# Performance work log

Measured on AMD Instinct MI355X. Metric: run time of the kernel, lower is better.

## Reference

```python
import jax, jax.numpy as jnp
import numpy as np

P, U, N = 1024, 196, 2048
B, T = 4, 512
D_IN, D_H, D_OUT = 384, 512, 256
NH, HD, TOPK = 4, 64, 64
EPS = 1e-5


def _ln(x, g, b):
    m = jnp.mean(x, axis=-1, keepdims=True)
    v = jnp.var(x, axis=-1, keepdims=True)
    return (x - m) * jax.lax.rsqrt(v + EPS) * g + b


def setup_inputs() -> dict:
    key = jax.random.key(0)
    k = jax.random.split(key, 12)
    s = 0.05
    return {
        'patches': jax.random.normal(k[0], (P, U, D_IN), jnp.float32),
        'patch_ids': jax.random.randint(k[1], (N,), 0, P),
        'valid_mask': jnp.ones((B, T), dtype=bool),
        'patch_center_gps': jax.random.normal(k[2], (N, 2), jnp.float32),
        'offsets': jax.random.randint(k[3], (N, 2), 0, 14),
        'W1': jax.random.normal(k[4], (D_IN, D_H), jnp.float32) * s,
        'b1': jnp.zeros((D_H,), jnp.float32),
        'W2': jax.random.normal(k[5], (D_H, D_OUT), jnp.float32) * s,
        'b2': jnp.zeros((D_OUT,), jnp.float32),
        'ln_q_g': jnp.ones((D_OUT,), jnp.float32),
        'ln_q_b': jnp.zeros((D_OUT,), jnp.float32),
        'ln_kv_g': jnp.ones((D_OUT,), jnp.float32),
        'ln_kv_b': jnp.zeros((D_OUT,), jnp.float32),
        'Wq': jax.random.normal(k[6], (D_OUT, D_OUT), jnp.float32) * s,
        'bq': jnp.zeros((D_OUT,), jnp.float32),
        'Wk': jax.random.normal(k[7], (D_OUT, D_OUT), jnp.float32) * s,
        'bk': jnp.zeros((D_OUT,), jnp.float32),
        'Wv': jax.random.normal(k[8], (D_OUT, D_OUT), jnp.float32) * s,
        'bv': jnp.zeros((D_OUT,), jnp.float32),
        'Wo': jax.random.normal(k[9], (D_OUT, D_OUT), jnp.float32) * s,
        'bo': jnp.zeros((D_OUT,), jnp.float32),
    }


def reference(patches, patch_ids, valid_mask, patch_center_gps, offsets,
              W1, b1, W2, b2, ln_q_g, ln_q_b, ln_kv_g, ln_kv_b,
              Wq, bq, Wk, bk, Wv, bv, Wo, bo):
    # gather patch feature grids per valid cell: [N, U, D_IN]
    gathered = patches[patch_ids]
    # adapter MLP (dropout is identity at eval)
    h = gathered @ W1 + b1
    h = jnp.where(h >= 0, h, 0.01 * h)  # LeakyReLU(0.01)
    a = h @ W2 + b2                      # [N, U, D_OUT]
    # offset-indexed query patch within the HxW grid
    Hs = int(np.sqrt(U)); Ws = Hs; ci = Hs // 2; cj = Ws // 2
    i_t = jnp.clip(ci + offsets[:, 1], 0, Hs - 1)
    j_t = jnp.clip(cj + offsets[:, 0], 0, Ws - 1)
    idx = (i_t * Ws + j_t).astype(jnp.int32)             # [N]
    query = jnp.take_along_axis(a, idx[:, None, None], axis=1)[:, 0]  # [N, D_OUT]
    # cosine similarity (F.normalize uses eps=1e-12 clamp on the norm)
    qn = query / jnp.clip(jnp.linalg.norm(query, axis=-1, keepdims=True), 1e-12)
    an = a / jnp.clip(jnp.linalg.norm(a, axis=-1, keepdims=True), 1e-12)
    sim = jnp.einsum('nd,nud->nu', qn, an)               # [N, U]
    _, topi = jax.lax.top_k(sim, TOPK)                   # [N, TOPK]
    kv = jnp.take_along_axis(a, topi[:, :, None], axis=1)  # [N, TOPK, D_OUT]
    # LayerNorm on q and kv, then multi-head cross-attention (1 query token)
    qln = _ln(query, ln_q_g, ln_q_b)
    kvln = _ln(kv, ln_kv_g, ln_kv_b)
    q = (qln @ Wq + bq).reshape(-1, NH, HD)              # [N, H, Hd]
    kk = (kvln @ Wk + bk).reshape(-1, TOPK, NH, HD)
    vv = (kvln @ Wv + bv).reshape(-1, TOPK, NH, HD)
    scores = jnp.einsum('nhd,nkhd->nhk', q, kk) / np.float32(np.sqrt(HD))
    w = jax.nn.softmax(scores, axis=-1)
    o = jnp.einsum('nhk,nkhd->nhd', w, vv).reshape(-1, D_OUT)
    attn = o @ Wo + bo                                   # [N, D_OUT]
    # masked scatter into [B, T, D_OUT] (row-major order of valid cells)
    mflat = valid_mask.reshape(-1)
    pos = jnp.cumsum(mflat.astype(jnp.int32)) - 1
    gath = attn[jnp.clip(pos, 0, attn.shape[0] - 1)]
    grid = jnp.where(mflat[:, None], gath, 0.0)
    return grid.reshape(valid_mask.shape[0], valid_mask.shape[1], D_OUT)
```

## Files before the change

kernel.cpp:

```cpp
#include <hip/hip_runtime.h>
#include <hip/hip_bf16.h>
#include <stdint.h>

#define NCELL 2048
#define UG    196
#define DIN   384
#define DH    512
#define DOUT  256
#define EPSV  1e-5f

typedef _Float16 f16;
typedef _Float16 f16x4 __attribute__((ext_vector_type(4)));
typedef _Float16 f16x8 __attribute__((ext_vector_type(8)));
typedef float    f32x16 __attribute__((ext_vector_type(16)));
typedef unsigned short ushortx4 __attribute__((ext_vector_type(4)));

#define AB_BYTES   205520896ull
#define QRAW_OFF   AB_BYTES
#define SIM_OFF    (QRAW_OFF + 2097152ull)
#define QNORM_OFF  (SIM_OFF + 1605632ull)
#define W1F_OFF    (QNORM_OFF + 8192ull)
#define W1F_BYTES  786432ull
#define W2F_OFF    (W1F_OFF + W1F_BYTES)
#define W2F_BYTES  524288ull

__global__ __launch_bounds__(256)
void k_prep(const float* __restrict__ W1, const float* __restrict__ W2,
            f16* __restrict__ w1f, f16* __restrict__ w2f)
{
    const int c = blockIdx.x * 256 + threadIdx.x;
    if (c < 49152) {
        const int lane = c & 63;
        const int part = (c >> 6) & 1;
        const int cg   = (c >> 7) & 7;
        const int half = (c >> 10) & 1;
        const int ks   = c >> 11;
        const int col  = (half * 8 + cg) * 32 + (lane & 31);
        const int kb   = ks * 16 + (lane >> 5) * 8;
        f16x8 o;
        #pragma unroll
        for (int j = 0; j < 8; ++j) {
            const float wv = W1[(size_t)(kb + j) * DH + col];
            const f16 hi = (f16)wv;
            o[j] = (part == 0) ? hi : (f16)(wv - (float)hi);
        }
        *(f16x8*)(w1f + (size_t)c * 8) = o;
    } else if (c < 81920) {
        const int c2 = c - 49152;
        const int lane = c2 & 63;
        const int part = (c2 >> 6) & 1;
        const int cg   = (c2 >> 7) & 7;
        const int ks   = c2 >> 10;
        const int col  = cg * 32 + (lane & 31);
        const int kb   = ks * 16 + (lane >> 5) * 8;
        f16x8 o;
        #pragma unroll
        for (int j = 0; j < 8; ++j) {
            const float wv = W2[(size_t)(kb + j) * DOUT + col];
            const f16 hi = (f16)wv;
            o[j] = (part == 0) ? hi : (f16)(wv - (float)hi);
        }
        *(f16x8*)(w2f + (size_t)c2 * 8) = o;
    }
}

__global__ __launch_bounds__(256)
void k_query(const float* __restrict__ patches, const int* __restrict__ patch_ids,
             const int* __restrict__ offsets,
             const float* __restrict__ W1, const float* __restrict__ b1,
             const float* __restrict__ W2, const float* __restrict__ b2,
             float* __restrict__ qraw, float* __restrict__ qnorm)
{
    __shared__ float sA[8 * DIN];
    __shared__ float sH[8 * DH];
    __shared__ float sPart[4 * 8];
    __shared__ int   sSrc[8];
    const int t  = threadIdx.x;
    const int nb = blockIdx.x * 8;
    if (t < 8) {
        int n  = nb + t;
        int ox = offsets[2 * n + 0];
        int oy = offsets[2 * n + 1];
        int it = min(max(7 + oy, 0), 13);
        int jt = min(max(7 + ox, 0), 13);
        sSrc[t] = patch_ids[n] * 196 + it * 14 + jt;
    }
    __syncthreads();
    #pragma unroll
    for (int i = 0; i < 3; ++i) {
        int fi = t + 256 * i;
        int r = fi / 96, c4 = fi % 96;
        const float4 v = ((const float4*)(patches + (size_t)sSrc[r] * DIN))[c4];
        ((float4*)(sA + r * DIN))[c4] = v;
    }
    __syncthreads();
    float h0[8], h1[8];
    {
        const float bb0 = b1[t], bb1 = b1[t + 256];
        #pragma unroll
        for (int r = 0; r < 8; ++r) { h0[r] = bb0; h1[r] = bb1; }
    }
    for (int k = 0; k < DIN; ++k) {
        const float w0 = W1[k * DH + t];
        const float w1 = W1[k * DH + t + 256];
        #pragma unroll
        for (int r = 0; r < 8; ++r) {
            const float av = sA[r * DIN + k];
            h0[r] = fmaf(av, w0, h0[r]);
            h1[r] = fmaf(av, w1, h1[r]);
        }
    }
    #pragma unroll
    for (int r = 0; r < 8; ++r) {
        float v0 = h0[r]; v0 = v0 >= 0.f ? v0 : 0.01f * v0;
        float v1 = h1[r]; v1 = v1 >= 0.f ? v1 : 0.01f * v1;
        sH[r * DH + t]       = v0;
        sH[r * DH + t + 256] = v1;
    }
    __syncthreads();
    float a8[8];
    {
        const float bb = b2[t];
        #pragma unroll
        for (int r = 0; r < 8; ++r) a8[r] = bb;
    }
    for (int k = 0; k < DH; ++k) {
        const float w = W2[k * DOUT + t];
        #pragma unroll
        for (int r = 0; r < 8; ++r) a8[r] = fmaf(sH[r * DH + k], w, a8[r]);
    }
    const int wid = t >> 6;
    #pragma unroll
    for (int r = 0; r < 8; ++r) {
        float p = a8[r] * a8[r];
        #pragma unroll
        for (int m = 1; m < 64; m <<= 1) p += __shfl_xor(p, m);
        if ((t & 63) == 0) sPart[wid * 8 + r] = p;
    }
    __syncthreads();
    if (t < 8) {
        float s = sPart[t] + sPart[8 + t] + sPart[16 + t] + sPart[24 + t];
        qnorm[nb + t] = fmaxf(sqrtf(s), 1e-12f);
    }
    #pragma unroll
    for (int r = 0; r < 8; ++r)
        qraw[(size_t)(nb + r) * DOUT + t] = a8[r];
}

__global__ __launch_bounds__(256)
void k_mlp(const float* __restrict__ patches, const int* __restrict__ patch_ids,
           const f16* __restrict__ w1f, const f16* __restrict__ w2f,
           const float* __restrict__ b1, const float* __restrict__ b2,
           const float* __restrict__ qraw, const float* __restrict__ qnorm,
           __hip_bfloat16* __restrict__ ab, float* __restrict__ sims)
{
    __shared__ __align__(16) unsigned char sAH[65536];
    __shared__ float sRed[256];
    const int t  = threadIdx.x;
    const int w  = t >> 6;
    const int l  = t & 63;
    const int R0 = blockIdx.x * 32;

    {
        const int row = t >> 3;
        const int Rg  = R0 + row;
        const int n   = Rg / UG, u = Rg - n * UG;
        const float* srcrow = patches + ((size_t)patch_ids[n] * UG + u) * DIN;
        const int swz = (row & 7) << 4;
        #pragma unroll
        for (int c = 0; c < 12; ++c) {
            const int k0 = (t & 7) * 4 + c * 32;
            const float4 v = *(const float4*)(srcrow + k0);
            f16x4 hi, lo;
            hi[0] = (f16)v.x; lo[0] = (f16)(v.x - (float)hi[0]);
            hi[1] = (f16)v.y; lo[1] = (f16)(v.y - (float)hi[1]);
            hi[2] = (f16)v.z; lo[2] = (f16)(v.z - (float)hi[2]);
            hi[3] = (f16)v.w; lo[3] = (f16)(v.w - (float)hi[3]);
            const int boff = row * 768 + ((k0 * 2) ^ swz);
            *(f16x4*)(sAH + boff)         = hi;
            *(f16x4*)(sAH + 24576 + boff) = lo;
        }
    }
    __syncthreads();

    f32x16 acc1[2][2];
    #pragma unroll
    for (int h = 0; h < 2; ++h)
        #pragma unroll
        for (int c = 0; c < 2; ++c)
            #pragma unroll
            for (int r = 0; r < 16; ++r) acc1[h][c][r] = 0.f;

    const int row  = l & 31;
    const int swzr = (row & 7) << 4;
    const f16* wb1 = w1f + (2 * w) * 1024 + l * 8;
    const f16* wb2 = w2f + (2 * w) * 1024 + l * 8;

#define LOADB(dst, base, s)                                   \
    {                                                         \
        const f16* bp_ = (base) + (size_t)(s) * 8192;         \
        dst##0 = *(const f16x8*)(bp_);                        \
        dst##1 = *(const f16x8*)(bp_ + 512);                  \
        dst##2 = *(const f16x8*)(bp_ + 1024);                 \
        dst##3 = *(const f16x8*)(bp_ + 1536);                 \
    }

#define STAGE1(s, B)                                                                  \
    {                                                                                 \
        const int ks_ = (s) >> 1, h_ = (s) & 1;                                       \
        const int aoff_ = row * 768 + ((ks_ * 32 + (l >> 5) * 16) ^ swzr);            \
        const f16x8 a_h = *(const f16x8*)(sAH + aoff_);                               \
        const f16x8 a_l = *(const f16x8*)(sAH + 24576 + aoff_);                       \
        acc1[h_][0] = __builtin_amdgcn_mfma_f32_32x32x16_f16(a_h, B##0, acc1[h_][0], 0, 0, 0); \
        acc1[h_][1] = __builtin_amdgcn_mfma_f32_32x32x16_f16(a_h, B##2, acc1[h_][1], 0, 0, 0); \
        acc1[h_][0] = __builtin_amdgcn_mfma_f32_32x32x16_f16(a_h, B##1, acc1[h_][0], 0, 0, 0); \
        acc1[h_][1] = __builtin_amdgcn_mfma_f32_32x32x16_f16(a_h, B##3, acc1[h_][1], 0, 0, 0); \
        acc1[h_][0] = __builtin_amdgcn_mfma_f32_32x32x16_f16(a_l, B##0, acc1[h_][0], 0, 0, 0); \
        acc1[h_][1] = __builtin_amdgcn_mfma_f32_32x32x16_f16(a_l, B##2, acc1[h_][1], 0, 0, 0); \
    }

    {
        f16x8 bA0, bA1, bA2, bA3, bB0, bB1, bB2, bB3;
        LOADB(bA, wb1, 0)
        for (int s2 = 0; s2 < 24; ++s2) {
            LOADB(bB, wb1, 2 * s2 + 1)
            STAGE1(2 * s2, bA)
            if (s2 < 23) LOADB(bA, wb1, 2 * s2 + 2)
            STAGE1(2 * s2 + 1, bB)
        }
    }
    __syncthreads();

    {
        #pragma unroll
        for (int h = 0; h < 2; ++h)
            #pragma unroll
            for (int c = 0; c < 2; ++c) {
                const int col = (h * 8 + 2 * w + c) * 32 + (l & 31);
                const float bb = b1[col];
                #pragma unroll
                for (int r = 0; r < 16; ++r) {
                    const int rw = (r & 3) + 8 * (r >> 2) + 4 * (l >> 5);
                    float v = acc1[h][c][r] + bb;
                    v = v >= 0.f ? v : 0.01f * v;
                    const f16 hh = (f16)v;
                    const f16 hl = (f16)(v - (float)hh);
                    const int boff = rw * 1024 + ((col * 2) ^ ((rw & 7) << 4));
                    *(f16*)(sAH + boff)         = hh;
                    *(f16*)(sAH + 32768 + boff) = hl;
                }
            }
    }
    __syncthreads();

    f32x16 acc2[2];
    #pragma unroll
    for (int c = 0; c < 2; ++c)
        #pragma unroll
        for (int r = 0; r < 16; ++r) acc2[c][r] = 0.f;

#define STAGE2(s, B)                                                                  \
    {                                                                                 \
        const int hoff_ = row * 1024 + (((s) * 32 + (l >> 5) * 16) ^ swzr);           \
        const f16x8 h_h = *(const f16x8*)(sAH + hoff_);                               \
        const f16x8 h_l = *(const f16x8*)(sAH + 32768 + hoff_);                       \
        acc2[0] = __builtin_amdgcn_mfma_f32_32x32x16_f16(h_h, B##0, acc2[0], 0, 0, 0); \
        acc2[1] = __builtin_amdgcn_mfma_f32_32x32x16_f16(h_h, B##2, acc2[1], 0, 0, 0); \
        acc2[0] = __builtin_amdgcn_mfma_f32_32x32x16_f16(h_h, B##1, acc2[0], 0, 0, 0); \
        acc2[1] = __builtin_amdgcn_mfma_f32_32x32x16_f16(h_h, B##3, acc2[1], 0, 0, 0); \
        acc2[0] = __builtin_amdgcn_mfma_f32_32x32x16_f16(h_l, B##0, acc2[0], 0, 0, 0); \
        acc2[1] = __builtin_amdgcn_mfma_f32_32x32x16_f16(h_l, B##2, acc2[1], 0, 0, 0); \
    }

    {
        f16x8 bA0, bA1, bA2, bA3, bB0, bB1, bB2, bB3;
        LOADB(bA, wb2, 0)
        for (int s2 = 0; s2 < 16; ++s2) {
            LOADB(bB, wb2, 2 * s2 + 1)
            STAGE2(2 * s2, bA)
            if (s2 < 15) LOADB(bA, wb2, 2 * s2 + 2)
            STAGE2(2 * s2 + 1, bB)
        }
    }
#undef LOADB
#undef STAGE1
#undef STAGE2

    float* sRedN = sRed;
    float* sRedD = sRed + 128;
    {
        float nrm[16], dot[16];
        #pragma unroll
        for (int r = 0; r < 16; ++r) { nrm[r] = 0.f; dot[r] = 0.f; }
        #pragma unroll
        for (int c = 0; c < 2; ++c) {
            const int col = (2 * w + c) * 32 + (l & 31);
            const float bb = b2[col];
            #pragma unroll
            for (int r = 0; r < 16; ++r) {
                const int rw = (r & 3) + 8 * (r >> 2) + 4 * (l >> 5);
                const int Rg = R0 + rw;
                const int n  = Rg / UG;
                const float a = acc2[c][r] + bb;
                const float q = qraw[(size_t)n * DOUT + col];
                nrm[r] = fmaf(a, a, nrm[r]);
                dot[r] = fmaf(a, q, dot[r]);
                ab[(size_t)Rg * DOUT + col] = __float2bfloat16(a);
            }
        }
        #pragma unroll
        for (int r = 0; r < 16; ++r) {
            #pragma unroll
            for (int m = 1; m < 32; m <<= 1) {
                nrm[r] += __shfl_xor(nrm[r], m);
                dot[r] += __shfl_xor(dot[r], m);
            }
        }
        if ((l & 31) == 0) {
            #pragma unroll
            for (int r = 0; r < 16; ++r) {
                const int rw = (r & 3) + 8 * (r >> 2) + 4 * (l >> 5);
                sRedN[rw * 4 + w] = nrm[r];
                sRedD[rw * 4 + w] = dot[r];
            }
        }
    }
    __syncthreads();
    if (t < 32) {
        const float nrm = sRedN[t * 4] + sRedN[t * 4 + 1] + sRedN[t * 4 + 2] + sRedN[t * 4 + 3];
        const float dot = sRedD[t * 4] + sRedD[t * 4 + 1] + sRedD[t * 4 + 2] + sRedD[t * 4 + 3];
        const int Rg = R0 + t, n = Rg / UG;
        sims[Rg] = dot / (qnorm[n] * fmaxf(sqrtf(nrm), 1e-12f));
    }
}

__global__ __launch_bounds__(256)
void k_attn(const __hip_bfloat16* __restrict__ ab,
            const float* __restrict__ qraw,
            const float* __restrict__ sims,
            const float* __restrict__ lnqg, const float* __restrict__ lnqb,
            const float* __restrict__ lnkg, const float* __restrict__ lnkb,
            const float* __restrict__ Wq, const float* __restrict__ bq,
            const float* __restrict__ Wk, const float* __restrict__ bk,
            const float* __restrict__ Wv, const float* __restrict__ bv,
            const float* __restrict__ Wo, const float* __restrict__ bo,
            float* __restrict__ out)
{
    __shared__ float sKV[64 * 257];
    __shared__ float ssim[256];
    __shared__ int   sflag[256];
    __shared__ int   ssel[64];
    __shared__ __align__(16) float sQln[256];
    __shared__ __align__(16) float sQp[256];
    __shared__ float sQw[4 * 256];
    __shared__ float sWatt[256];
    __shared__ float sWkv[4 * 256];
    __shared__ float sO[256];
    __shared__ float sred[8];

    const int t = threadIdx.x;
    const int n = blockIdx.x;
    (void)bk;

    ssim[t] = (t < 196) ? sims[(size_t)n * 196 + t] : -3.0e38f;
    const float qv = qraw[(size_t)n * DOUT + t];
    float s1 = qv, s2 = qv * qv;
    #pragma unroll
    for (int m = 1; m < 64; m <<= 1) { s1 += __shfl_xor(s1, m); s2 += __shfl_xor(s2, m); }
    if ((t & 63) == 0) { sred[t >> 6] = s1; sred[4 + (t >> 6)] = s2; }
    __syncthreads();
    {
        const float mean = (sred[0] + sred[1] + sred[2] + sred[3]) * (1.f / 256.f);
        const float var  = (sred[4] + sred[5] + sred[6] + sred[7]) * (1.f / 256.f) - mean * mean;
        sQln[t] = (qv - mean) * rsqrtf(var + EPSV) * lnqg[t] + lnqb[t];
    }
    int flag = 0;
    if (t < 196) {
        const float su = ssim[t];
        int rank = 0;
        for (int v = 0; v < 196; ++v) {
            const float sv = ssim[v];
            rank += (sv > su) || (sv == su && v < t);
        }
        flag = (rank < 64) ? 1 : 0;
    }
    sflag[t] = flag;
    __syncthreads();
    if (flag) {
        int pos = 0;
        for (int v = 0; v < t; ++v) pos += sflag[v];
        ssel[pos] = t;
    }
    __syncthreads();

    {
        float acc = bq[t];
        for (int k = 0; k < 256; ++k)
            acc = fmaf(sQln[k], Wq[k * DOUT + t], acc);
        sQp[t] = acc;
    }

    {
        const int s = t >> 2;
        const int q = t & 3;
        const int u = ssel[s];
        const unsigned short* src =
            (const unsigned short*)(ab + ((size_t)n * 196 + u) * (size_t)DOUT);
        float sum = 0.f, ssq = 0.f;
        #pragma unroll
        for (int i = 0; i < 16; ++i) {
            const int c = q * 4 + i * 16;
            const ushortx4 rv = *(const ushortx4*)(src + c);
            #pragma unroll
            for (int j = 0; j < 4; ++j) {
                const float f = __builtin_bit_cast(float, (unsigned)rv[j] << 16);
                sKV[s * 257 + c + j] = f;
                sum += f; ssq = fmaf(f, f, ssq);
            }
        }
        sum += __shfl_xor(sum, 1); ssq += __shfl_xor(ssq, 1);
        sum += __shfl_xor(sum, 2); ssq += __shfl_xor(ssq, 2);
        const float mean = sum * (1.f / 256.f);
        const float inv  = rsqrtf(ssq * (1.f / 256.f) - mean * mean + EPSV);
        #pragma unroll
        for (int i = 0; i < 16; ++i) {
            const int c = q * 4 + i * 16;
            const float4 g = *(const float4*)(lnkg + c);
            const float4 b = *(const float4*)(lnkb + c);
            float x0 = sKV[s * 257 + c + 0], x1 = sKV[s * 257 + c + 1];
            float x2 = sKV[s * 257 + c + 2], x3 = sKV[s * 257 + c + 3];
            sKV[s * 257 + c + 0] = (x0 - mean) * inv * g.x + b.x;
            sKV[s * 257 + c + 1] = (x1 - mean) * inv * g.y + b.y;
            sKV[s * 257 + c + 2] = (x2 - mean) * inv * g.z + b.z;
            sKV[s * 257 + c + 3] = (x3 - mean) * inv * g.w + b.w;
        }
    }
    __syncthreads();

    {
        const float* wrow = Wk + (size_t)t * DOUT;
        #pragma unroll
        for (int h = 0; h < 4; ++h) {
            float acc = 0.f;
            #pragma unroll
            for (int d4 = 0; d4 < 16; ++d4) {
                const float4 wv = *(const float4*)(wrow + h * 64 + d4 * 4);
                const float4 qp = *(const float4*)(sQp + h * 64 + d4 * 4);
                acc = fmaf(qp.x, wv.x, acc);
                acc = fmaf(qp.y, wv.y, acc);
                acc = fmaf(qp.z, wv.z, acc);
                acc = fmaf(qp.w, wv.w, acc);
            }
            sQw[h * 256 + t] = acc;
        }
    }
    __syncthreads();

    {
        const int h = t >> 6, s = t & 63;
        float acc = 0.f;
        for (int k = 0; k < 256; ++k)
            acc = fmaf(sKV[s * 257 + k], sQw[h * 256 + k], acc);
        float sc = acc * 0.125f;
        float mx = sc;
        #pragma unroll
        for (int m = 1; m < 64; m <<= 1) mx = fmaxf(mx, __shfl_xor(mx, m));
        const float e = expf(sc - mx);
        float sum = e;
        #pragma unroll
        for (int m = 1; m < 64; m <<= 1) sum += __shfl_xor(sum, m);
        sWatt[t] = e / sum;
    }
    __syncthreads();

    {
        float a0 = 0.f, a1 = 0.f, a2 = 0.f, a3 = 0.f;
        for (int s = 0; s < 64; ++s) {
            const float kvv = sKV[s * 257 + t];
            a0 = fmaf(sWatt[s], kvv, a0);
            a1 = fmaf(sWatt[64 + s], kvv, a1);
            a2 = fmaf(sWatt[128 + s], kvv, a2);
            a3 = fmaf(sWatt[192 + s], kvv, a3);
        }
        sWkv[t] = a0; sWkv[256 + t] = a1; sWkv[512 + t] = a2; sWkv[768 + t] = a3;
    }
    __syncthreads();

    {
        const int h = t >> 6;
        float acc = bv[t];
        for (int k = 0; k < 256; ++k)
            acc = fmaf(sWkv[h * 256 + k], Wv[k * DOUT + t], acc);
        sO[t] = acc;
    }
    __syncthreads();

    {
        float acc = bo[t];
        for (int k = 0; k < 256; ++k)
            acc = fmaf(sO[k], Wo[k * DOUT + t], acc);
        out[(size_t)n * DOUT + t] = acc;
    }
}

extern "C" void kernel_launch(void* const* d_in, const int* in_sizes, int n_in,
                              void* d_out, int out_size, void* d_ws, size_t ws_size,
                              hipStream_t stream) {
    (void)in_sizes; (void)n_in; (void)out_size; (void)ws_size;
    const float* patches   = (const float*)d_in[0];
    const int*   patch_ids = (const int*)d_in[1];
    const int*   offsets   = (const int*)d_in[4];
    const float* W1 = (const float*)d_in[5];
    const float* b1 = (const float*)d_in[6];
    const float* W2 = (const float*)d_in[7];
    const float* b2 = (const float*)d_in[8];
    const float* lnqg = (const float*)d_in[9];
    const float* lnqb = (const float*)d_in[10];
    const float* lnkg = (const float*)d_in[11];
    const float* lnkb = (const float*)d_in[12];
    const float* Wq = (const float*)d_in[13];
    const float* bq = (const float*)d_in[14];
    const float* Wk = (const float*)d_in[15];
    const float* bk = (const float*)d_in[16];
    const float* Wv = (const float*)d_in[17];
    const float* bv = (const float*)d_in[18];
    const float* Wo = (const float*)d_in[19];
    const float* bo = (const float*)d_in[20];

    uint8_t* ws = (uint8_t*)d_ws;
    __hip_bfloat16* ab    = (__hip_bfloat16*)(ws);
    float*          qraw  = (float*)(ws + QRAW_OFF);
    float*          sims  = (float*)(ws + SIM_OFF);
    float*          qnorm = (float*)(ws + QNORM_OFF);
    f16*            w1f   = (f16*)(ws + W1F_OFF);
    f16*            w2f   = (f16*)(ws + W2F_OFF);
    float*          out   = (float*)d_out;

    hipLaunchKernelGGL(k_prep, dim3(320), dim3(256), 0, stream, W1, W2, w1f, w2f);
    hipLaunchKernelGGL(k_query, dim3(NCELL / 8), dim3(256), 0, stream,
                       patches, patch_ids, offsets, W1, b1, W2, b2, qraw, qnorm);
    hipLaunchKernelGGL(k_mlp, dim3((NCELL * UG) / 32), dim3(256), 0, stream,
                       patches, patch_ids, w1f, w2f, b1, b2, qraw, qnorm, ab, sims);
    hipLaunchKernelGGL(k_attn, dim3(NCELL), dim3(256), 0, stream,
                       ab, qraw, sims, lnqg, lnqb, lnkg, lnkb,
                       Wq, bq, Wk, bk, Wv, bv, Wo, bo, out);
}
```

Baseline: 1.212 ms.

## Use 8 waves per k_mlp block, halving per-wave column tiles

Measured after the change: 1.127 ms. -7.0%, faster.

```diff
diff --git a/kernel.cpp b/kernel.cpp
--- a/kernel.cpp
+++ b/kernel.cpp
@@ -147,7 +147,7 @@
         qraw[(size_t)(nb + r) * DOUT + t] = a8[r];
 }
 
-__global__ __launch_bounds__(256)
+__global__ __launch_bounds__(512)
 void k_mlp(const float* __restrict__ patches, const int* __restrict__ patch_ids,
            const f16* __restrict__ w1f, const f16* __restrict__ w2f,
            const float* __restrict__ b1, const float* __restrict__ b2,
@@ -155,21 +155,21 @@
            __hip_bfloat16* __restrict__ ab, float* __restrict__ sims)
 {
     __shared__ __align__(16) unsigned char sAH[65536];
-    __shared__ float sRed[256];
+    __shared__ float sRed[512];
     const int t  = threadIdx.x;
     const int w  = t >> 6;
     const int l  = t & 63;
     const int R0 = blockIdx.x * 32;
 
     {
-        const int row = t >> 3;
+        const int row = t >> 4;
         const int Rg  = R0 + row;
         const int n   = Rg / UG, u = Rg - n * UG;
         const float* srcrow = patches + ((size_t)patch_ids[n] * UG + u) * DIN;
         const int swz = (row & 7) << 4;
         #pragma unroll
-        for (int c = 0; c < 12; ++c) {
-            const int k0 = (t & 7) * 4 + c * 32;
+        for (int c = 0; c < 6; ++c) {
+            const int k0 = (t & 15) * 4 + c * 64;
             const float4 v = *(const float4*)(srcrow + k0);
             f16x4 hi, lo;
             hi[0] = (f16)v.x; lo[0] = (f16)(v.x - (float)hi[0]);
@@ -181,132 +181,127 @@
             *(f16x4*)(sAH + 24576 + boff) = lo;
         }
     }
-    __syncthreads();
-
-    f32x16 acc1[2][2];
-    #pragma unroll
-    for (int h = 0; h < 2; ++h)
-        #pragma unroll
-        for (int c = 0; c < 2; ++c)
-            #pragma unroll
-            for (int r = 0; r < 16; ++r) acc1[h][c][r] = 0.f;
 
     const int row  = l & 31;
     const int swzr = (row & 7) << 4;
-    const f16* wb1 = w1f + (2 * w) * 1024 + l * 8;
-    const f16* wb2 = w2f + (2 * w) * 1024 + l * 8;
-
-#define LOADB(dst, base, s)                                   \
-    {                                                         \
-        const f16* bp_ = (base) + (size_t)(s) * 8192;         \
-        dst##0 = *(const f16x8*)(bp_);                        \
-        dst##1 = *(const f16x8*)(bp_ + 512);                  \
-        dst##2 = *(const f16x8*)(bp_ + 1024);                 \
-        dst##3 = *(const f16x8*)(bp_ + 1536);                 \
-    }
-
-#define STAGE1(s, B)                                                                  \
-    {                                                                                 \
-        const int ks_ = (s) >> 1, h_ = (s) & 1;                                       \
-        const int aoff_ = row * 768 + ((ks_ * 32 + (l >> 5) * 16) ^ swzr);            \
-        const f16x8 a_h = *(const f16x8*)(sAH + aoff_);                               \
-        const f16x8 a_l = *(const f16x8*)(sAH + 24576 + aoff_);                       \
-        acc1[h_][0] = __builtin_amdgcn_mfma_f32_32x32x16_f16(a_h, B##0, acc1[h_][0], 0, 0, 0); \
-        acc1[h_][1] = __builtin_amdgcn_mfma_f32_32x32x16_f16(a_h, B##2, acc1[h_][1], 0, 0, 0); \
-        acc1[h_][0] = __builtin_amdgcn_mfma_f32_32x32x16_f16(a_h, B##1, acc1[h_][0], 0, 0, 0); \
-        acc1[h_][1] = __builtin_amdgcn_mfma_f32_32x32x16_f16(a_h, B##3, acc1[h_][1], 0, 0, 0); \
-        acc1[h_][0] = __builtin_amdgcn_mfma_f32_32x32x16_f16(a_l, B##0, acc1[h_][0], 0, 0, 0); \
-        acc1[h_][1] = __builtin_amdgcn_mfma_f32_32x32x16_f16(a_l, B##2, acc1[h_][1], 0, 0, 0); \
-    }
-
-    {
-        f16x8 bA0, bA1, bA2, bA3, bB0, bB1, bB2, bB3;
-        LOADB(bA, wb1, 0)
-        for (int s2 = 0; s2 < 24; ++s2) {
-            LOADB(bB, wb1, 2 * s2 + 1)
-            STAGE1(2 * s2, bA)
-            if (s2 < 23) LOADB(bA, wb1, 2 * s2 + 2)
-            STAGE1(2 * s2 + 1, bB)
-        }
-    }
-    __syncthreads();
-
-    {
-        #pragma unroll
-        for (int h = 0; h < 2; ++h)
-            #pragma unroll
-            for (int c = 0; c < 2; ++c) {
-                const int col = (h * 8 + 2 * w + c) * 32 + (l & 31);
-                const float bb = b1[col];
-                #pragma unroll
-                for (int r = 0; r < 16; ++r) {
-                    const int rw = (r & 3) + 8 * (r >> 2) + 4 * (l >> 5);
-                    float v = acc1[h][c][r] + bb;
-                    v = v >= 0.f ? v : 0.01f * v;
-                    const f16 hh = (f16)v;
-                    const f16 hl = (f16)(v - (float)hh);
-                    const int boff = rw * 1024 + ((col * 2) ^ ((rw & 7) << 4));
-                    *(f16*)(sAH + boff)         = hh;
-                    *(f16*)(sAH + 32768 + boff) = hl;
-                }
-            }
-    }
-    __syncthreads();
-
-    f32x16 acc2[2];
-    #pragma unroll
-    for (int c = 0; c < 2; ++c)
-        #pragma unroll
-        for (int r = 0; r < 16; ++r) acc2[c][r] = 0.f;
-
-#define STAGE2(s, B)                                                                  \
-    {                                                                                 \
-        const int hoff_ = row * 1024 + (((s) * 32 + (l >> 5) * 16) ^ swzr);           \
-        const f16x8 h_h = *(const f16x8*)(sAH + hoff_);                               \
-        const f16x8 h_l = *(const f16x8*)(sAH + 32768 + hoff_);                       \
-        acc2[0] = __builtin_amdgcn_mfma_f32_32x32x16_f16(h_h, B##0, acc2[0], 0, 0, 0); \
-        acc2[1] = __builtin_amdgcn_mfma_f32_32x32x16_f16(h_h, B##2, acc2[1], 0, 0, 0); \
-        acc2[0] = __builtin_amdgcn_mfma_f32_32x32x16_f16(h_h, B##1, acc2[0], 0, 0, 0); \
-        acc2[1] = __builtin_amdgcn_mfma_f32_32x32x16_f16(h_h, B##3, acc2[1], 0, 0, 0); \
-        acc2[0] = __builtin_amdgcn_mfma_f32_32x32x16_f16(h_l, B##0, acc2[0], 0, 0, 0); \
-        acc2[1] = __builtin_amdgcn_mfma_f32_32x32x16_f16(h_l, B##2, acc2[1], 0, 0, 0); \
-    }
-
-    {
-        f16x8 bA0, bA1, bA2, bA3, bB0, bB1, bB2, bB3;
-        LOADB(bA, wb2, 0)
-        for (int s2 = 0; s2 < 16; ++s2) {
-            LOADB(bB, wb2, 2 * s2 + 1)
-            STAGE2(2 * s2, bA)
-            if (s2 < 15) LOADB(bA, wb2, 2 * s2 + 2)
-            STAGE2(2 * s2 + 1, bB)
-        }
-    }
-#undef LOADB
-#undef STAGE1
-#undef STAGE2
-
-    float* sRedN = sRed;
-    float* sRedD = sRed + 128;
-    {
-        float nrm[16], dot[16];
-        #pragma unroll
-        for (int r = 0; r < 16; ++r) { nrm[r] = 0.f; dot[r] = 0.f; }
-        #pragma unroll
-        for (int c = 0; c < 2; ++c) {
-            const int col = (2 * w + c) * 32 + (l & 31);
-            const float bb = b2[col];
+    const f16* wb1 = w1f + w * 1024 + l * 8;
+    const f16* wb2 = w2f + w * 1024 + l * 8;
+
+    f32x16 acc1[2];
+    #pragma unroll
+    for (int h = 0; h < 2; ++h)
+        #pragma unroll
+        for (int r = 0; r < 16; ++r) acc1[h][r] = 0.f;
+
+#define LOADK(A0, A1, A2, A3, ks_)                              \
+    {                                                           \
+        const f16* bp_ = wb1 + (size_t)(ks_) * 16384;           \
+        A0 = *(const f16x8*)(bp_);                              \
+        A1 = *(const f16x8*)(bp_ + 512);                        \
+        A2 = *(const f16x8*)(bp_ + 8192);                       \
+        A3 = *(const f16x8*)(bp_ + 8192 + 512);                 \
+    }
+
+#define KSTEP(ks_, B0, B1, B2, B3)                                                     \
+    {                                                                                  \
+        const int aoff_ = row * 768 + (((ks_) * 32 + (l >> 5) * 16) ^ swzr);           \
+        const f16x8 a_h = *(const f16x8*)(sAH + aoff_);                                \
+        const f16x8 a_l = *(const f16x8*)(sAH + 24576 + aoff_);                        \
+        acc1[0] = __builtin_amdgcn_mfma_f32_32x32x16_f16(a_h, B0, acc1[0], 0, 0, 0);   \
+        acc1[1] = __builtin_amdgcn_mfma_f32_32x32x16_f16(a_h, B2, acc1[1], 0, 0, 0);   \
+        acc1[0] = __builtin_amdgcn_mfma_f32_32x32x16_f16(a_h, B1, acc1[0], 0, 0, 0);   \
+        acc1[1] = __builtin_amdgcn_mfma_f32_32x32x16_f16(a_h, B3, acc1[1], 0, 0, 0);   \
+        acc1[0] = __builtin_amdgcn_mfma_f32_32x32x16_f16(a_l, B0, acc1[0], 0, 0, 0);   \
+        acc1[1] = __builtin_amdgcn_mfma_f32_32x32x16_f16(a_l, B2, acc1[1], 0, 0, 0);   \
+    }
+
+    {
+        f16x8 P0, P1, P2, P3, Q0, Q1, Q2, Q3;
+        LOADK(P0, P1, P2, P3, 0)
+        __syncthreads();
+        for (int it = 0; it < 12; ++it) {
+            const int ks = 2 * it;
+            LOADK(Q0, Q1, Q2, Q3, ks + 1)
+            KSTEP(ks, P0, P1, P2, P3)
+            if (it < 11) LOADK(P0, P1, P2, P3, ks + 2)
+            KSTEP(ks + 1, Q0, Q1, Q2, Q3)
+        }
+    }
+    __syncthreads();
+
+    {
+        #pragma unroll
+        for (int h = 0; h < 2; ++h) {
+            const int col = (h * 8 + w) * 32 + (l & 31);
+            const float bb = b1[col];
             #pragma unroll
             for (int r = 0; r < 16; ++r) {
                 const int rw = (r & 3) + 8 * (r >> 2) + 4 * (l >> 5);
-                const int Rg = R0 + rw;
-                const int n  = Rg / UG;
-                const float a = acc2[c][r] + bb;
-                const float q = qraw[(size_t)n * DOUT + col];
-                nrm[r] = fmaf(a, a, nrm[r]);
-                dot[r] = fmaf(a, q, dot[r]);
-                ab[(size_t)Rg * DOUT + col] = __float2bfloat16(a);
+                float v = acc1[h][r] + bb;
+                v = v >= 0.f ? v : 0.01f * v;
+                const f16 hh = (f16)v;
+                const f16 hl = (f16)(v - (float)hh);
+                const int boff = rw * 1024 + ((col * 2) ^ ((rw & 7) << 4));
+                *(f16*)(sAH + boff)         = hh;
+                *(f16*)(sAH + 32768 + boff) = hl;
             }
+        }
+    }
+
+    f32x16 acc2;
+    #pragma unroll
+    for (int r = 0; r < 16; ++r) acc2[r] = 0.f;
+
+#define LOADS2(A0, A1, s_)                                      \
+    {                                                           \
+        const f16* bp_ = wb2 + (size_t)(s_) * 8192;             \
+        A0 = *(const f16x8*)(bp_);                              \
+        A1 = *(const f16x8*)(bp_ + 512);                        \
+    }
+
+#define S2STEP(s_, B0, B1)                                                             \
+    {                                                                                  \
+        const int hoff_ = row * 1024 + (((s_) * 32 + (l >> 5) * 16) ^ swzr);           \
+        const f16x8 h_h = *(const f16x8*)(sAH + hoff_);                                \
+        const f16x8 h_l = *(const f16x8*)(sAH + 32768 + hoff_);                        \
+        acc2 = __builtin_amdgcn_mfma_f32_32x32x16_f16(h_h, B0, acc2, 0, 0, 0);         \
+        acc2 = __builtin_amdgcn_mfma_f32_32x32x16_f16(h_h, B1, acc2, 0, 0, 0);         \
+        acc2 = __builtin_amdgcn_mfma_f32_32x32x16_f16(h_l, B0, acc2, 0, 0, 0);         \
+    }
+
+    {
+        f16x8 P0, P1, Q0, Q1;
+        LOADS2(P0, P1, 0)
+        __syncthreads();
+        for (int it = 0; it < 16; ++it) {
+            const int s = 2 * it;
+            LOADS2(Q0, Q1, s + 1)
+            S2STEP(s, P0, P1)
+            if (it < 15) LOADS2(P0, P1, s + 2)
+            S2STEP(s + 1, Q0, Q1)
+        }
+    }
+#undef LOADK
+#undef KSTEP
+#undef LOADS2
+#undef S2STEP
+
+    float* sRedN = sRed;
+    float* sRedD = sRed + 256;
+    {
+        const int col = w * 32 + (l & 31);
+        const float bb = b2[col];
+        float nrm[16], dot[16];
+        #pragma unroll
+        for (int r = 0; r < 16; ++r) {
+            const int rw = (r & 3) + 8 * (r >> 2) + 4 * (l >> 5);
+            const int Rg = R0 + rw;
+            const int n  = Rg / UG;
+            const float a = acc2[r] + bb;
+            const float q = qraw[(size_t)n * DOUT + col];
+            nrm[r] = a * a;
+            dot[r] = a * q;
+            ab[(size_t)Rg * DOUT + col] = __float2bfloat16(a);
         }
         #pragma unroll
         for (int r = 0; r < 16; ++r) {
@@ -320,15 +315,16 @@
             #pragma unroll
             for (int r = 0; r < 16; ++r) {
                 const int rw = (r & 3) + 8 * (r >> 2) + 4 * (l >> 5);
-                sRedN[rw * 4 + w] = nrm[r];
-                sRedD[rw * 4 + w] = dot[r];
+                sRedN[rw * 8 + w] = nrm[r];
+                sRedD[rw * 8 + w] = dot[r];
             }
         }
     }
     __syncthreads();
     if (t < 32) {
-        const float nrm = sRedN[t * 4] + sRedN[t * 4 + 1] + sRedN[t * 4 + 2] + sRedN[t * 4 + 3];
-        const float dot = sRedD[t * 4] + sRedD[t * 4 + 1] + sRedD[t * 4 + 2] + sRedD[t * 4 + 3];
+        float nrm = 0.f, dot = 0.f;
+        #pragma unroll
+        for (int j = 0; j < 8; ++j) { nrm += sRedN[t * 8 + j]; dot += sRedD[t * 8 + j]; }
         const int Rg = R0 + t, n = Rg / UG;
         sims[Rg] = dot / (qnorm[n] * fmaxf(sqrtf(nrm), 1e-12f));
     }
@@ -539,7 +535,7 @@
     hipLaunchKernelGGL(k_prep, dim3(320), dim3(256), 0, stream, W1, W2, w1f, w2f);
     hipLaunchKernelGGL(k_query, dim3(NCELL / 8), dim3(256), 0, stream,
                        patches, patch_ids, offsets, W1, b1, W2, b2, qraw, qnorm);
-    hipLaunchKernelGGL(k_mlp, dim3((NCELL * UG) / 32), dim3(256), 0, stream,
+    hipLaunchKernelGGL(k_mlp, dim3((NCELL * UG) / 32), dim3(512), 0, stream,
                        patches, patch_ids, w1f, w2f, b1, b2, qraw, qnorm, ab, sims);
     hipLaunchKernelGGL(k_attn, dim3(NCELL), dim3(256), 0, stream,
                        ab, qraw, sims, lnqg, lnqb, lnkg, lnkb,
```
